# Optimization experiments

Hardware: AMD Instinct MI355X
Metric: run time of the kernel (lower is better)

## Reference

```python
import jax, jax.numpy as jnp
import numpy as np

# model dims
VOCAB = 32000; D = 256; FF = 1024; L = 2; NH = 8; HD_ATT = D // NH; T_MAX = 128
# memory bank dims
SLOTS = 512; MD = 128; MH = 4; HD = MD // MH; TOPK = 8
B = 4; T = 128


def _ln(x, g, b):
    m = x.mean(-1, keepdims=True)
    v = x.var(-1, keepdims=True)
    return (x - m) * jax.lax.rsqrt(v + 1e-5) * g + b


def _topk_softmax(scores, k):
    # sparse addressing: softmax restricted to the top-k slots per head
    vals = jax.lax.top_k(scores, k)[0]
    thr = vals[..., -1:]
    neg = jnp.finfo(scores.dtype).min
    return jax.nn.softmax(jnp.where(scores >= thr, scores, neg), axis=-1)


def setup_inputs() -> dict:
    key = jax.random.key(0)
    ks = jax.random.split(key, 12)
    s = 0.02
    return {
        "input_seq": jax.random.randint(ks[0], (B, T), 0, VOCAB),
        "tok_emb": jax.random.normal(ks[1], (VOCAB, D)) * s,
        "pos_emb": jax.random.normal(ks[2], (T_MAX, D)) * s,
        "Wqkv": jax.random.normal(ks[3], (L, D, 3 * D)) * s,
        "Wo": jax.random.normal(ks[4], (L, D, D)) * s,
        "ln1_g": jnp.ones((L, D)), "ln1_b": jnp.zeros((L, D)),
        "ln2_g": jnp.ones((L, D)), "ln2_b": jnp.zeros((L, D)),
        "W1": jax.random.normal(ks[5], (L, D, FF)) * s, "b1": jnp.zeros((L, FF)),
        "W2": jax.random.normal(ks[6], (L, FF, D)) * s, "b2": jnp.zeros((L, D)),
        "lnf_g": jnp.ones((D,)), "lnf_b": jnp.zeros((D,)),
        "W_logits": jax.random.normal(ks[7], (D + MD, VOCAB)) * s,
        "b_logits": jnp.zeros((VOCAB,)),
        "W_iface": jax.random.normal(ks[8], (D + MD, MH * (4 * HD + 1))) * s,
        "b_iface": jnp.zeros((MH * (4 * HD + 1),)),
        "beta_read": jnp.asarray(1.0), "beta_write": jnp.asarray(1.0),
    }


def _forward(input_seq, tok_emb, pos_emb, Wqkv, Wo, ln1_g, ln1_b, ln2_g, ln2_b,
             W1, b1, W2, b2, lnf_g, lnf_b, W_logits, b_logits, W_iface, b_iface,
             beta_read, beta_write):
    Bc, Tc = input_seq.shape
    x = tok_emb[input_seq] + pos_emb[:Tc]  # [B,T,D]
    neg = jnp.finfo(x.dtype).min
    causal = jnp.tril(jnp.ones((Tc, Tc), bool))
    for l in range(L):  # small fixed layer count
        h = _ln(x, ln1_g[l], ln1_b[l])
        q, k, v = jnp.split(h @ Wqkv[l], 3, axis=-1)
        q = q.reshape(Bc, Tc, NH, HD_ATT)
        k = k.reshape(Bc, Tc, NH, HD_ATT)
        v = v.reshape(Bc, Tc, NH, HD_ATT)
        att = jnp.einsum('bqhd,bkhd->bhqk', q, k) / np.sqrt(HD_ATT)
        att = jax.nn.softmax(jnp.where(causal, att, neg), axis=-1)
        o = jnp.einsum('bhqk,bkhd->bqhd', att, v).reshape(Bc, Tc, D)
        x = x + o @ Wo[l]
        h = _ln(x, ln2_g[l], ln2_b[l])
        x = x + jax.nn.gelu(h @ W1[l] + b1[l]) @ W2[l] + b2[l]
    x = _ln(x, lnf_g, lnf_b)  # causal controller states h_t for every prefix

    beta_r = jnp.clip(jax.nn.softplus(beta_read), 1.0, 20.0)
    beta_w = jnp.clip(jax.nn.softplus(beta_write), 1.0, 20.0)
    M0 = jnp.zeros((Bc, MH, SLOTS, HD), x.dtype)
    rv0 = jnp.zeros((Bc, MD), x.dtype)

    def step(carry, h_t):
        M, rv = carry
        c = jnp.concatenate([h_t, rv], axis=-1)  # [B, D+MD]
        logits_t = c @ W_logits + b_logits
        iface = (c @ W_iface + b_iface).reshape(Bc, MH, 4 * HD + 1)
        rk = iface[..., 0 * HD:1 * HD]
        wk = iface[..., 1 * HD:2 * HD]
        wv = iface[..., 2 * HD:3 * HD]
        erase = jax.nn.sigmoid(iface[..., 3 * HD:4 * HD])
        add_gate = jax.nn.sigmoid(iface[..., 4 * HD:])  # [B,MH,1]
        # read (topk content addressing), accumulate into read_vec
        w_r = _topk_softmax(jnp.einsum('bhd,bhsd->bhs', rk, M) * beta_r, TOPK)
        rv = rv + jnp.einsum('bhs,bhsd->bhd', w_r, M).reshape(Bc, MD)
        # write with erase/add gating
        w_w = _topk_softmax(jnp.einsum('bhd,bhsd->bhs', wk, M) * beta_w, TOPK)
        M = M * (1.0 - w_w[..., None] * erase[:, :, None, :]) \
            + (add_gate * w_w)[..., None] * wv[:, :, None, :]
        return (M, rv), logits_t

    _, logits = jax.lax.scan(step, (M0, rv0), jnp.swapaxes(x, 0, 1))
    return jnp.swapaxes(logits, 0, 1)  # [B,T,VOCAB]


def reference(input_seq, tok_emb, pos_emb, Wqkv, Wo, ln1_g, ln1_b, ln2_g, ln2_b,
              W1, b1, W2, b2, lnf_g, lnf_b, W_logits, b_logits, W_iface, b_iface,
              beta_read, beta_write):
    return _forward(input_seq, tok_emb, pos_emb, Wqkv, Wo, ln1_g, ln1_b, ln2_g,
                    ln2_b, W1, b1, W2, b2, lnf_g, lnf_b, W_logits, b_logits,
                    W_iface, b_iface, beta_read, beta_write)
```

## Files before the change

### kernel.cpp

```cpp
#include <hip/hip_runtime.h>
#include <hip/hip_bf16.h>
#include <math.h>

typedef __bf16 bf16;
typedef __bf16 bf16x8 __attribute__((ext_vector_type(8)));
typedef float f32x4 __attribute__((ext_vector_type(4)));
typedef float f32x16 __attribute__((ext_vector_type(16)));

#define B_ 4
#define T_ 128
#define D_ 256
#define FF_ 1024
#define HD_ 32
#define VOCAB_ 32000
#define NC_ 516
#define KBIG_ 384

struct TJob { const float* src; bf16* dst; int K; int N; int blk0; };
struct TJobs { TJob j[9]; };
__global__ __launch_bounds__(256) void k_tr_embed(TJobs js, const int* __restrict__ ids,
                                                  const float* __restrict__ tok,
                                                  const float* __restrict__ pos,
                                                  const float* __restrict__ g,
                                                  const float* __restrict__ b,
                                                  float* __restrict__ X, bf16* __restrict__ out,
                                                  unsigned* __restrict__ flags) {
    int bid = blockIdx.x;
    if (bid == 0 && threadIdx.x == 0) flags[0] = 0u;
    if (bid < 420) {
        __shared__ float tile[64][65];
        int r = 0;
#pragma unroll
        for (int i = 1; i < 9; i++) if (bid >= js.j[i].blk0) r = i;
        TJob jb = js.j[r];
        int local = bid - jb.blk0;
        int tiles_k = jb.K >> 6;
        int ik = local % tiles_k, in = local / tiles_k;
        int k0 = ik * 64, n0 = in * 64;
        int tx = threadIdx.x & 63, ty = threadIdx.x >> 6;
#pragma unroll
        for (int rr = 0; rr < 64; rr += 4) {
            int kk = k0 + rr + ty, nn = n0 + tx;
            tile[rr + ty][tx] = (nn < jb.N) ? jb.src[(size_t)kk * jb.N + nn] : 0.f;
        }
        __syncthreads();
#pragma unroll
        for (int rr = 0; rr < 64; rr += 4) {
            int nn = n0 + rr + ty, kk = k0 + tx;
            jb.dst[(size_t)nn * jb.K + kk] = (bf16)tile[tx][rr + ty];
        }
        return;
    }
    int row = bid - 420;
    int d   = threadIdx.x;
    int t   = row & (T_ - 1);
    int id  = ids[row];
    float v = tok[(size_t)id * D_ + d] + pos[(size_t)t * D_ + d];
    X[(size_t)row * D_ + d] = v;
    float s1 = v, s2 = v * v;
#pragma unroll
    for (int off = 32; off > 0; off >>= 1) {
        s1 += __shfl_xor(s1, off);
        s2 += __shfl_xor(s2, off);
    }
    __shared__ float r1[4], r2[4];
    int wid = d >> 6, lane = d & 63;
    if (lane == 0) { r1[wid] = s1; r2[wid] = s2; }
    __syncthreads();
    float tot1 = r1[0] + r1[1] + r1[2] + r1[3];
    float tot2 = r2[0] + r2[1] + r2[2] + r2[3];
    float mean = tot1 * (1.f / D_);
    float var  = tot2 * (1.f / D_) - mean * mean;
    float rs   = rsqrtf(var + 1e-5f);
    out[(size_t)row * D_ + d] = (bf16)((v - mean) * rs * g[d] + b[d]);
}

__global__ void k_ln(const float* __restrict__ X, const float* __restrict__ g,
                     const float* __restrict__ b, bf16* __restrict__ out, int ostride) {
    int row = blockIdx.x;
    int d   = threadIdx.x;
    float v = X[(size_t)row * D_ + d];
    float s1 = v, s2 = v * v;
#pragma unroll
    for (int off = 32; off > 0; off >>= 1) {
        s1 += __shfl_xor(s1, off);
        s2 += __shfl_xor(s2, off);
    }
    __shared__ float r1[4], r2[4];
    int wid = d >> 6, lane = d & 63;
    if (lane == 0) { r1[wid] = s1; r2[wid] = s2; }
    __syncthreads();
    float tot1 = r1[0] + r1[1] + r1[2] + r1[3];
    float tot2 = r2[0] + r2[1] + r2[2] + r2[3];
    float mean = tot1 * (1.f / D_);
    float var  = tot2 * (1.f / D_) - mean * mean;
    float rs   = rsqrtf(var + 1e-5f);
    out[(size_t)row * ostride + d] = (bf16)((v - mean) * rs * g[d] + b[d]);
}

template <bool BIAS, bool GELU_, bool RESID, bool OBF16>
__global__ __launch_bounds__(256) void k_dgemm(const bf16* __restrict__ A, int lda,
                                               const bf16* __restrict__ BT,
                                               const float* __restrict__ bias,
                                               float* __restrict__ Cf, bf16* __restrict__ Cb,
                                               int ldc, int N, int K) {
    int tid = threadIdx.x;
    int lane = tid & 63, wid = tid >> 6;
    int wm = wid >> 1, wn = wid & 1;
    int m0 = blockIdx.y * 64, n0 = blockIdx.x * 64;
    int r = lane & 15, q = lane >> 4;

    const bf16* Ab = A  + (size_t)(m0 + wm * 32 + r) * lda + q * 8;
    const bf16* Bb = BT + (size_t)(n0 + wn * 32 + r) * K   + q * 8;

    f32x4 acc[2][2] = {};
#pragma unroll 4
    for (int k0 = 0; k0 < K; k0 += 32) {
        bf16x8 a0 = *(const bf16x8*)(Ab + k0);
        bf16x8 a1 = *(const bf16x8*)(Ab + (size_t)16 * lda + k0);
        bf16x8 b0 = *(const bf16x8*)(Bb + k0);
        bf16x8 b1 = *(const bf16x8*)(Bb + (size_t)16 * K + k0);
        acc[0][0] = __builtin_amdgcn_mfma_f32_16x16x32_bf16(a0, b0, acc[0][0], 0, 0, 0);
        acc[0][1] = __builtin_amdgcn_mfma_f32_16x16x32_bf16(a0, b1, acc[0][1], 0, 0, 0);
        acc[1][0] = __builtin_amdgcn_mfma_f32_16x16x32_bf16(a1, b0, acc[1][0], 0, 0, 0);
        acc[1][1] = __builtin_amdgcn_mfma_f32_16x16x32_bf16(a1, b1, acc[1][1], 0, 0, 0);
    }

#pragma unroll
    for (int mi = 0; mi < 2; mi++) {
#pragma unroll
        for (int ni = 0; ni < 2; ni++) {
            int col = n0 + wn * 32 + ni * 16 + r;
            if (col < N) {
                int rowb = m0 + wm * 32 + mi * 16 + (q << 2);
                float bsv = BIAS ? bias[col] : 0.f;
#pragma unroll
                for (int j = 0; j < 4; j++) {
                    float val = acc[mi][ni][j] + bsv;
                    if (GELU_) {
                        float u = val;
                        val = 0.5f * u * (1.f + tanhf(0.7978845608028654f * (u + 0.044715f * u * u * u)));
                    }
                    size_t idx = (size_t)(rowb + j) * ldc + col;
                    if (RESID) Cf[idx] += val;
                    else if (OBF16) Cb[idx] = (bf16)val;
                    else Cf[idx] = val;
                }
            }
        }
    }
}

__global__ __launch_bounds__(256) void k_attn(const float* __restrict__ QKV, bf16* __restrict__ O) {
    __shared__ __align__(16) bf16 Qs[128][40];
    __shared__ __align__(16) bf16 Ks[128][40];
    __shared__ __align__(16) bf16 VT[32][136];
    __shared__ __align__(16) bf16 PT[128][136];
    __shared__ float Ls[128];
    int tid = threadIdx.x;
    int lane = tid & 63, w = tid >> 6;
    int l5 = lane >> 5, l31 = lane & 31;
    int b = blockIdx.x >> 3, h = blockIdx.x & 7;

    {
        int t = tid & 127, half = tid >> 7, d0 = half * 16;
        size_t rowb = (size_t)(b * T_ + t) * 768 + h * HD_ + d0;
        bf16 tq[16], tk[16];
#pragma unroll
        for (int i4 = 0; i4 < 4; i4++) {
            float4 qv = *(const float4*)&QKV[rowb + 4 * i4];
            float4 kv = *(const float4*)&QKV[rowb + 256 + 4 * i4];
            float4 vv = *(const float4*)&QKV[rowb + 512 + 4 * i4];
            tq[4 * i4] = (bf16)qv.x; tq[4 * i4 + 1] = (bf16)qv.y; tq[4 * i4 + 2] = (bf16)qv.z; tq[4 * i4 + 3] = (bf16)qv.w;
            tk[4 * i4] = (bf16)kv.x; tk[4 * i4 + 1] = (bf16)kv.y; tk[4 * i4 + 2] = (bf16)kv.z; tk[4 * i4 + 3] = (bf16)kv.w;
            VT[d0 + 4 * i4][t]     = (bf16)vv.x;
            VT[d0 + 4 * i4 + 1][t] = (bf16)vv.y;
            VT[d0 + 4 * i4 + 2][t] = (bf16)vv.z;
            VT[d0 + 4 * i4 + 3][t] = (bf16)vv.w;
        }
        *(bf16x8*)&Qs[t][d0]     = *(bf16x8*)&tq[0];
        *(bf16x8*)&Qs[t][d0 + 8] = *(bf16x8*)&tq[8];
        *(bf16x8*)&Ks[t][d0]     = *(bf16x8*)&tk[0];
        *(bf16x8*)&Ks[t][d0 + 8] = *(bf16x8*)&tk[8];
    }
    __syncthreads();

    const float scale = 0.17677669529663687f;
#pragma unroll
    for (int qt = 0; qt < 4; qt++) {
        f32x16 acc = {};
        bf16x8 a0 = *(const bf16x8*)&Ks[32 * w + l31][8 * l5];
        bf16x8 b0 = *(const bf16x8*)&Qs[32 * qt + l31][8 * l5];
        acc = __builtin_amdgcn_mfma_f32_32x32x16_bf16(a0, b0, acc, 0, 0, 0);
        bf16x8 a1 = *(const bf16x8*)&Ks[32 * w + l31][16 + 8 * l5];
        bf16x8 b1 = *(const bf16x8*)&Qs[32 * qt + l31][16 + 8 * l5];
        acc = __builtin_amdgcn_mfma_f32_32x32x16_bf16(a1, b1, acc, 0, 0, 0);
        int qg = 32 * qt + l31;
#pragma unroll
        for (int r = 0; r < 16; r++) {
            int key = 32 * w + (r & 3) + 8 * (r >> 2) + 4 * l5;
            float p = (key <= qg) ? expf(acc[r] * scale) : 0.f;
            PT[qg][key] = (bf16)p;
        }
    }
    __syncthreads();

    if (tid < 128) {
        float s = 0.f;
#pragma unroll
        for (int kk = 0; kk < 128; kk += 8) {
            bf16x8 v = *(const bf16x8*)&PT[tid][kk];
#pragma unroll
            for (int j = 0; j < 8; j++) s += (float)v[j];
        }
        Ls[tid] = 1.f / s;
    }

    f32x16 oacc = {};
#pragma unroll
    for (int kap = 0; kap < 8; kap++) {
        bf16x8 af = *(const bf16x8*)&PT[32 * w + l31][16 * kap + 8 * l5];
        bf16x8 bv = *(const bf16x8*)&VT[l31][16 * kap + 8 * l5];
        oacc = __builtin_amdgcn_mfma_f32_32x32x16_bf16(af, bv, oacc, 0, 0, 0);
    }
    __syncthreads();
#pragma unroll
    for (int r = 0; r < 16; r++) {
        int qg = 32 * w + (r & 3) + 8 * (r >> 2) + 4 * l5;
        O[(size_t)(b * T_ + qg) * D_ + h * HD_ + l31] = (bf16)(oacc[r] * Ls[qg]);
    }
}

union SPool {
    struct { bf16 rvh[T_][128]; __align__(16) bf16 rvb[2][128]; } scan;
    struct { __align__(16) bf16 BsT[64][392]; } log;
};

__global__ __launch_bounds__(256) void k_scan_logits(const float* __restrict__ Wif,
                                                     const float* __restrict__ HIF,
                                                     bf16* __restrict__ Abig,
                                                     const float* __restrict__ Bm,
                                                     const float* __restrict__ bias,
                                                     float* __restrict__ C,
                                                     unsigned* __restrict__ flags) {
    __shared__ SPool sp;
    int tid = threadIdx.x;
    int lane = tid & 63, w = tid >> 6;

    if (blockIdx.x < 4) {
        int b = blockIdx.x;
        int r = lane & 15, q = lane >> 4;
        int d = lane & 31;

        bf16x8 bfrag[5][4];
#pragma unroll
        for (int ti = 0; ti < 5; ti++) {
#pragma unroll
            for (int kap = 0; kap < 4; kap++) {
                bf16x8 v;
#pragma unroll
                for (int j = 0; j < 8; j++) {
                    int k = 32 * kap + 8 * q + j;
                    float wv_ = 0.f;
                    if (ti < 4) {
                        int fl = w * 129 + 64 + 16 * ti + r;
                        wv_ = Wif[(size_t)(256 + k) * NC_ + fl];
                    } else if (r == 0) {
                        wv_ = Wif[(size_t)(256 + k) * NC_ + (w * 129 + 128)];
                    }
                    v[j] = (bf16)wv_;
                }
                bfrag[ti][kap] = v;
            }
        }

        const float* HB = HIF + (size_t)(b * T_) * NC_ + w * 129;
        float hw_n = HB[64 + d], he_n = HB[96 + d], ha_n = HB[128];

        if (tid < 128) sp.scan.rvb[0][tid] = (bf16)0.f;
        float rv1 = 0.f, mm1 = 0.f;
        __syncthreads();

        for (int t = 0; t < T_; t++) {
            const bf16* rb = &sp.scan.rvb[t & 1][0];
            bf16x8 afr0 = *(const bf16x8*)&rb[8 * q];
            bf16x8 afr1 = *(const bf16x8*)&rb[32 + 8 * q];
            bf16x8 afr2 = *(const bf16x8*)&rb[64 + 8 * q];
            bf16x8 afr3 = *(const bf16x8*)&rb[96 + 8 * q];

            float hw = hw_n, he = he_n, ha = ha_n;
            if (t + 1 < T_) {
                const float* Hr = HB + (size_t)(t + 1) * NC_;
                hw_n = Hr[64 + d]; he_n = Hr[96 + d]; ha_n = Hr[128];
            }

            float tv[5];
#pragma unroll
            for (int ti = 0; ti < 5; ti++) {
                f32x4 a0 = {}, a1 = {};
                a0 = __builtin_amdgcn_mfma_f32_16x16x32_bf16(afr0, bfrag[ti][0], a0, 0, 0, 0);
                a1 = __builtin_amdgcn_mfma_f32_16x16x32_bf16(afr1, bfrag[ti][1], a1, 0, 0, 0);
                a0 = __builtin_amdgcn_mfma_f32_16x16x32_bf16(afr2, bfrag[ti][2], a0, 0, 0, 0);
                a1 = __builtin_amdgcn_mfma_f32_16x16x32_bf16(afr3, bfrag[ti][3], a1, 0, 0, 0);
                tv[ti] = a0[0] + a1[0];
            }
            float wv0 = __shfl(tv[0], r), wv1 = __shfl(tv[1], r);
            float er0 = __shfl(tv[2], r), er1 = __shfl(tv[3], r);
            float gv  = __shfl(tv[4], 0);
            float gw = (d < 16) ? wv0 : wv1;
            float ge = (d < 16) ? er0 : er1;

            if (lane < 32) {
                float gwv = gw + hw;
                float gev = ge + he;
                float gav = gv + ha;
                float er = 1.f / (1.f + expf(-gev));
                float ag = 1.f / (1.f + expf(-gav));
                sp.scan.rvh[t][32 * w + d] = (bf16)rv1;
                float mn = mm1 * (1.f - er * (1.f / 512.f)) + ag * (1.f / 512.f) * gwv;
                rv1 += mm1;
                mm1 = mn;
                sp.scan.rvb[(t + 1) & 1][32 * w + d] = (bf16)rv1;
            }
            __syncthreads();
        }

        for (int idx = tid; idx < T_ * 128; idx += 256) {
            int t = idx >> 7, dd = idx & 127;
            Abig[(size_t)(b * T_ + t) * KBIG_ + 256 + dd] = sp.scan.rvh[t][dd];
        }
        __threadfence();
        __syncthreads();
        if (tid == 0) atomicAdd(&flags[0], 1u);
        return;
    }

    int wm = w >> 1, wn = w & 1;
    int n0 = (blockIdx.x - 4) * 64;

    int bn = tid & 63, bk = (tid >> 6) << 3;
#pragma unroll
    for (int k0 = 0; k0 < KBIG_; k0 += 32) {
        bf16x8 bv;
#pragma unroll
        for (int e = 0; e < 8; e++) bv[e] = (bf16)Bm[(size_t)(k0 + bk + e) * VOCAB_ + n0 + bn];
        *(bf16x8*)&sp.log.BsT[bn][k0 + bk] = bv;
    }

    float bsv[2];
#pragma unroll
    for (int ni = 0; ni < 2; ni++) bsv[ni] = bias[n0 + wn * 32 + ni * 16 + (lane & 15)];

    if (tid == 0) {
        while (atomicAdd(&flags[0], 0u) < 4u) __builtin_amdgcn_s_sleep(32);
    }
    __syncthreads();
    __threadfence();

    const bf16* A = Abig;
    int kfrag = (lane >> 4) << 3;
    for (int mt = 0; mt < 8; mt++) {
        int m0 = mt * 64;
        f32x4 acc[2][2] = {};
#pragma unroll
        for (int kk = 0; kk < KBIG_; kk += 32) {
            bf16x8 af[2], bfv[2];
#pragma unroll
            for (int mi = 0; mi < 2; mi++)
                af[mi] = *(const bf16x8*)&A[(size_t)(m0 + wm * 32 + mi * 16 + (lane & 15)) * KBIG_ + kk + kfrag];
#pragma unroll
            for (int ni = 0; ni < 2; ni++)
                bfv[ni] = *(const bf16x8*)&sp.log.BsT[wn * 32 + ni * 16 + (lane & 15)][kk + kfrag];
#pragma unroll
            for (int mi = 0; mi < 2; mi++)
#pragma unroll
                for (int ni = 0; ni < 2; ni++)
                    acc[mi][ni] = __builtin_amdgcn_mfma_f32_16x16x32_bf16(af[mi], bfv[ni], acc[mi][ni], 0, 0, 0);
        }
#pragma unroll
        for (int mi = 0; mi < 2; mi++) {
#pragma unroll
            for (int ni = 0; ni < 2; ni++) {
                int colg = n0 + wn * 32 + ni * 16 + (lane & 15);
                int rowb = m0 + wm * 32 + mi * 16 + ((lane >> 4) << 2);
#pragma unroll
                for (int j = 0; j < 4; j++)
                    C[(size_t)(rowb + j) * VOCAB_ + colg] = acc[mi][ni][j] + bsv[ni];
            }
        }
    }
}

extern "C" void kernel_launch(void* const* d_in, const int* in_sizes, int n_in,
                              void* d_out, int out_size, void* d_ws, size_t ws_size,
                              hipStream_t stream) {
    const int*   ids  = (const int*)d_in[0];
    const float* tok  = (const float*)d_in[1];
    const float* pos  = (const float*)d_in[2];
    const float* Wqkv = (const float*)d_in[3];
    const float* Wo   = (const float*)d_in[4];
    const float* ln1g = (const float*)d_in[5];
    const float* ln1b = (const float*)d_in[6];
    const float* ln2g = (const float*)d_in[7];
    const float* ln2b = (const float*)d_in[8];
    const float* W1   = (const float*)d_in[9];
    const float* b1   = (const float*)d_in[10];
    const float* W2   = (const float*)d_in[11];
    const float* b2   = (const float*)d_in[12];
    const float* lnfg = (const float*)d_in[13];
    const float* lnfb = (const float*)d_in[14];
    const float* Wl   = (const float*)d_in[15];
    const float* bl   = (const float*)d_in[16];
    const float* Wif  = (const float*)d_in[17];
    const float* bif  = (const float*)d_in[18];

    char* ws = (char*)d_ws;
    float* X    = (float*)(ws + 0);
    float* QKV  = (float*)(ws + 524288);
    bf16*  Hb   = (bf16*)(ws + 2097152);
    bf16*  Obf  = (bf16*)(ws + 2359296);
    bf16*  FF1  = (bf16*)(ws + 2621440);
    float* HIF  = (float*)(ws + 3670016);
    bf16*  Abig = (bf16*)(ws + 4726784);
    bf16*  WqkvT= (bf16*)(ws + 5120000);
    bf16*  WoT  = (bf16*)(ws + 5906432);
    bf16*  W1T  = (bf16*)(ws + 6168576);
    bf16*  W2T  = (bf16*)(ws + 7217152);
    bf16*  WifT = (bf16*)(ws + 8265728);
    unsigned* flags = (unsigned*)(ws + 8560640);
    float* outp = (float*)d_out;

    TJobs js;
    int blk = 0;
    auto setj = [&](int i, const float* s, bf16* d, int K, int N, int Npad) {
        js.j[i] = {s, d, K, N, blk};
        blk += (K >> 6) * (Npad >> 6);
    };
    setj(0, Wqkv,              WqkvT,              256, 768, 768);
    setj(1, Wqkv + 256 * 768,  WqkvT + 768 * 256,  256, 768, 768);
    setj(2, Wo,                WoT,                256, 256, 256);
    setj(3, Wo + 256 * 256,    WoT + 256 * 256,    256, 256, 256);
    setj(4, W1,                W1T,                256, 1024, 1024);
    setj(5, W1 + 256 * 1024,   W1T + 1024 * 256,   256, 1024, 1024);
    setj(6, W2,                W2T,                1024, 256, 256);
    setj(7, W2 + 1024 * 256,   W2T + 256 * 1024,   1024, 256, 256);
    setj(8, Wif,               WifT,               256, NC_, 576);

    k_tr_embed<<<blk + 512, 256, 0, stream>>>(js, ids, tok, pos, ln1g, ln1b, X, Hb, flags);

    for (int l = 0; l < 2; l++) {
        k_dgemm<false, false, false, false><<<dim3(12, 8), 256, 0, stream>>>(
            Hb, D_, WqkvT + (size_t)l * 768 * 256, nullptr, QKV, nullptr, 768, 768, 256);
        k_attn<<<32, 256, 0, stream>>>(QKV, Obf);
        k_dgemm<false, false, true, false><<<dim3(4, 8), 256, 0, stream>>>(
            Obf, D_, WoT + (size_t)l * 256 * 256, nullptr, X, nullptr, D_, D_, 256);
        k_ln<<<512, 256, 0, stream>>>(X, ln2g + l * D_, ln2b + l * D_, Hb, D_);
        k_dgemm<true, true, false, true><<<dim3(16, 8), 256, 0, stream>>>(
            Hb, D_, W1T + (size_t)l * 1024 * 256, b1 + l * FF_, nullptr, FF1, FF_, FF_, 256);
        k_dgemm<true, false, true, false><<<dim3(4, 8), 256, 0, stream>>>(
            FF1, FF_, W2T + (size_t)l * 256 * 1024, b2 + l * D_, X, nullptr, D_, D_, 1024);
        if (l == 0)
            k_ln<<<512, 256, 0, stream>>>(X, ln1g + D_, ln1b + D_, Hb, D_);
    }

    k_ln<<<512, 256, 0, stream>>>(X, lnfg, lnfb, Abig, KBIG_);
    k_dgemm<true, false, false, false><<<dim3(9, 8), 256, 0, stream>>>(
        Abig, KBIG_, WifT, bif, HIF, nullptr, NC_, NC_, 256);
    k_scan_logits<<<504, 256, 0, stream>>>(Wif, HIF, Abig, Wl, bl, outp, flags);
}
```

Measured before the change: 283.1 us.

## Overlap logits GEMM K<256 with memory scan; stream read vectors directly

The logits blocks now compute the first 256 K columns (transformer hidden part, which does not depend on the scan) before waiting on the scan-completion flag, keeping all 8 M-tiles of accumulators in registers, then finish the last 128 K columns after the flag. The scan blocks write read vectors straight to global memory each step instead of staging them in LDS and copying at the end, and replace __syncthreads with a lighter lgkmcnt wait plus s_barrier. This hides most GEMM work behind the serial scan, at the cost of 128 accumulator registers per thread, which may reduce occupancy or cause spills.

```diff
diff --git a/kernel.cpp b/kernel.cpp
--- a/kernel.cpp
+++ b/kernel.cpp
@@ -232,7 +232,7 @@
 }
 
 union SPool {
-    struct { bf16 rvh[T_][128]; __align__(16) bf16 rvb[2][128]; } scan;
+    struct { __align__(16) bf16 rvb[2][128]; } scan;
     struct { __align__(16) bf16 BsT[64][392]; } log;
 };
 
@@ -276,23 +276,24 @@
 
         const float* HB = HIF + (size_t)(b * T_) * NC_ + w * 129;
         float hw_n = HB[64 + d], he_n = HB[96 + d], ha_n = HB[128];
+        bf16* Aout = Abig + 256 + 32 * w + d;
 
         if (tid < 128) sp.scan.rvb[0][tid] = (bf16)0.f;
         float rv1 = 0.f, mm1 = 0.f;
         __syncthreads();
 
         for (int t = 0; t < T_; t++) {
+            float hw = hw_n, he = he_n, ha = ha_n;
+            if (t + 1 < T_) {
+                const float* Hr = HB + (size_t)(t + 1) * NC_;
+                hw_n = Hr[64 + d]; he_n = Hr[96 + d]; ha_n = Hr[128];
+            }
+
             const bf16* rb = &sp.scan.rvb[t & 1][0];
             bf16x8 afr0 = *(const bf16x8*)&rb[8 * q];
             bf16x8 afr1 = *(const bf16x8*)&rb[32 + 8 * q];
             bf16x8 afr2 = *(const bf16x8*)&rb[64 + 8 * q];
             bf16x8 afr3 = *(const bf16x8*)&rb[96 + 8 * q];
-
-            float hw = hw_n, he = he_n, ha = ha_n;
-            if (t + 1 < T_) {
-                const float* Hr = HB + (size_t)(t + 1) * NC_;
-                hw_n = Hr[64 + d]; he_n = Hr[96 + d]; ha_n = Hr[128];
-            }
 
             float tv[5];
 #pragma unroll
@@ -316,19 +317,18 @@
                 float gav = gv + ha;
                 float er = 1.f / (1.f + expf(-gev));
                 float ag = 1.f / (1.f + expf(-gav));
-                sp.scan.rvh[t][32 * w + d] = (bf16)rv1;
+                Aout[(size_t)(b * T_ + t) * KBIG_] = (bf16)rv1;
                 float mn = mm1 * (1.f - er * (1.f / 512.f)) + ag * (1.f / 512.f) * gwv;
                 rv1 += mm1;
                 mm1 = mn;
                 sp.scan.rvb[(t + 1) & 1][32 * w + d] = (bf16)rv1;
             }
-            __syncthreads();
-        }
-
-        for (int idx = tid; idx < T_ * 128; idx += 256) {
-            int t = idx >> 7, dd = idx & 127;
-            Abig[(size_t)(b * T_ + t) * KBIG_ + 256 + dd] = sp.scan.rvh[t][dd];
-        }
+            asm volatile("s_waitcnt lgkmcnt(0)" ::: "memory");
+            __builtin_amdgcn_s_barrier();
+            __builtin_amdgcn_sched_barrier(0);
+        }
+
+        asm volatile("s_waitcnt vmcnt(0)" ::: "memory");
         __threadfence();
         __syncthreads();
         if (tid == 0) atomicAdd(&flags[0], 1u);
@@ -337,6 +337,8 @@
 
     int wm = w >> 1, wn = w & 1;
     int n0 = (blockIdx.x - 4) * 64;
+    int rr = lane & 15, q = lane >> 4;
+    int kfrag = q << 3;
 
     int bn = tid & 63, bk = (tid >> 6) << 3;
 #pragma unroll
@@ -346,10 +348,34 @@
         for (int e = 0; e < 8; e++) bv[e] = (bf16)Bm[(size_t)(k0 + bk + e) * VOCAB_ + n0 + bn];
         *(bf16x8*)&sp.log.BsT[bn][k0 + bk] = bv;
     }
+    __syncthreads();
 
     float bsv[2];
 #pragma unroll
-    for (int ni = 0; ni < 2; ni++) bsv[ni] = bias[n0 + wn * 32 + ni * 16 + (lane & 15)];
+    for (int ni = 0; ni < 2; ni++) bsv[ni] = bias[n0 + wn * 32 + ni * 16 + rr];
+
+    const bf16* A = Abig;
+    f32x4 acc[8][2][2] = {};
+
+#pragma unroll
+    for (int kk = 0; kk < 256; kk += 32) {
+        bf16x8 bfv[2];
+#pragma unroll
+        for (int ni = 0; ni < 2; ni++)
+            bfv[ni] = *(const bf16x8*)&sp.log.BsT[wn * 32 + ni * 16 + rr][kk + kfrag];
+#pragma unroll
+        for (int mt = 0; mt < 8; mt++) {
+            bf16x8 af[2];
+#pragma unroll
+            for (int mi = 0; mi < 2; mi++)
+                af[mi] = *(const bf16x8*)&A[(size_t)(mt * 64 + wm * 32 + mi * 16 + rr) * KBIG_ + kk + kfrag];
+#pragma unroll
+            for (int mi = 0; mi < 2; mi++)
+#pragma unroll
+                for (int ni = 0; ni < 2; ni++)
+                    acc[mt][mi][ni] = __builtin_amdgcn_mfma_f32_16x16x32_bf16(af[mi], bfv[ni], acc[mt][mi][ni], 0, 0, 0);
+        }
+    }
 
     if (tid == 0) {
         while (atomicAdd(&flags[0], 0u) < 4u) __builtin_amdgcn_s_sleep(32);
@@ -357,35 +383,37 @@
     __syncthreads();
     __threadfence();
 
-    const bf16* A = Abig;
-    int kfrag = (lane >> 4) << 3;
+#pragma unroll
+    for (int kk = 256; kk < KBIG_; kk += 32) {
+        bf16x8 bfv[2];
+#pragma unroll
+        for (int ni = 0; ni < 2; ni++)
+            bfv[ni] = *(const bf16x8*)&sp.log.BsT[wn * 32 + ni * 16 + rr][kk + kfrag];
+#pragma unroll
+        for (int mt = 0; mt < 8; mt++) {
+            bf16x8 af[2];
+#pragma unroll
+            for (int mi = 0; mi < 2; mi++)
+                af[mi] = *(const bf16x8*)&A[(size_t)(mt * 64 + wm * 32 + mi * 16 + rr) * KBIG_ + kk + kfrag];
+#pragma unroll
+            for (int mi = 0; mi < 2; mi++)
+#pragma unroll
+                for (int ni = 0; ni < 2; ni++)
+                    acc[mt][mi][ni] = __builtin_amdgcn_mfma_f32_16x16x32_bf16(af[mi], bfv[ni], acc[mt][mi][ni], 0, 0, 0);
+        }
+    }
+
+#pragma unroll
     for (int mt = 0; mt < 8; mt++) {
-        int m0 = mt * 64;
-        f32x4 acc[2][2] = {};
-#pragma unroll
-        for (int kk = 0; kk < KBIG_; kk += 32) {
-            bf16x8 af[2], bfv[2];
-#pragma unroll
-            for (int mi = 0; mi < 2; mi++)
-                af[mi] = *(const bf16x8*)&A[(size_t)(m0 + wm * 32 + mi * 16 + (lane & 15)) * KBIG_ + kk + kfrag];
-#pragma unroll
-            for (int ni = 0; ni < 2; ni++)
-                bfv[ni] = *(const bf16x8*)&sp.log.BsT[wn * 32 + ni * 16 + (lane & 15)][kk + kfrag];
-#pragma unroll
-            for (int mi = 0; mi < 2; mi++)
-#pragma unroll
-                for (int ni = 0; ni < 2; ni++)
-                    acc[mi][ni] = __builtin_amdgcn_mfma_f32_16x16x32_bf16(af[mi], bfv[ni], acc[mi][ni], 0, 0, 0);
-        }
 #pragma unroll
         for (int mi = 0; mi < 2; mi++) {
 #pragma unroll
             for (int ni = 0; ni < 2; ni++) {
-                int colg = n0 + wn * 32 + ni * 16 + (lane & 15);
-                int rowb = m0 + wm * 32 + mi * 16 + ((lane >> 4) << 2);
+                int colg = n0 + wn * 32 + ni * 16 + rr;
+                int rowb = mt * 64 + wm * 32 + mi * 16 + (q << 2);
 #pragma unroll
                 for (int j = 0; j < 4; j++)
-                    C[(size_t)(rowb + j) * VOCAB_ + colg] = acc[mi][ni][j] + bsv[ni];
+                    C[(size_t)(rowb + j) * VOCAB_ + colg] = acc[mt][mi][ni][j] + bsv[ni];
             }
         }
     }
```

After: 277.5 us. 2.0% less time.
